# Kernel tuning notes

Hardware: AMD Instinct MI355X
Metric: run time of the kernel (lower is better)

Reference implementation:

```python
import jax, jax.numpy as jnp
import numpy as np

BATCH = 4096
NUM_INPUTS = 784
WIDTH = 16000        # neurons per logic layer, divisible by NUM_CLASSES
N_HIDDEN = 4         # width->width layers stacked for scan (plus the input layer)
NUM_CLASSES = 10


def setup_inputs() -> dict:
    key = jax.random.key(0)
    ks = jax.random.split(key, 7)
    x = jax.random.bernoulli(ks[0], 0.5, (BATCH, NUM_INPUTS))
    idx_a0 = jax.random.randint(ks[1], (WIDTH,), 0, NUM_INPUTS, dtype=jnp.int32)
    idx_b0 = jax.random.randint(ks[2], (WIDTH,), 0, NUM_INPUTS, dtype=jnp.int32)
    neg0 = jax.random.bernoulli(ks[3], 0.5, (WIDTH, 2))
    idx_a = jax.random.randint(ks[4], (N_HIDDEN, WIDTH), 0, WIDTH, dtype=jnp.int32)
    idx_b = jax.random.randint(ks[5], (N_HIDDEN, WIDTH), 0, WIDTH, dtype=jnp.int32)
    neg = jax.random.bernoulli(ks[6], 0.5, (N_HIDDEN, WIDTH, 2))
    return {"x": x, "idx_a0": idx_a0, "idx_b0": idx_b0, "neg0": neg0,
            "idx_a": idx_a, "idx_b": idx_b, "neg": neg}


def _gate(a, b, nf):
    # gate = (maybe-NOT a) AND (maybe-NOT b); NOT on booleans == XOR with flag
    return (a ^ nf[:, 0]) & (b ^ nf[:, 1])


def reference(x, idx_a0, idx_b0, neg0, idx_a, idx_b, neg):
    # input layer: gather wires from the boolean input
    h = _gate(x[:, idx_a0], x[:, idx_b0], neg0)  # [BATCH, WIDTH] bool

    def step(h, p):
        ia, ib, nf = p
        return _gate(h[:, ia], h[:, ib], nf), None

    h, _ = jax.lax.scan(step, h, (idx_a, idx_b, neg))
    # GroupSum: popcount per class group -> int32 logits
    out = h.reshape(BATCH, NUM_CLASSES, WIDTH // NUM_CLASSES).sum(-1, dtype=jnp.int32)
    return out
```

## Files before the change

### kernel.cpp

```cpp
#include <hip/hip_runtime.h>


#define NIN   784
#define WIDTH 16000
#define SW    16384
#define NH    4
#define NC    10
#define GPC   1600
#define NBLK  128
#define TPB   1024

typedef unsigned int u32;

__global__ void desc_kernel(const int* __restrict__ ia0, const int* __restrict__ ib0,
                            const int* __restrict__ n0,
                            const int* __restrict__ ia, const int* __restrict__ ib,
                            const int* __restrict__ n, u32* __restrict__ desc) {
    int t = blockIdx.x * blockDim.x + threadIdx.x;
    if (t >= (NH + 1) * SW) return;
    int l = t >> 14;
    int g = t & (SW - 1);
    u32 d = 0;
    if (g < WIDTH) {
        int a, b, na, nb;
        if (l == 0) { a = ia0[g]; b = ib0[g]; na = n0[2 * g]; nb = n0[2 * g + 1]; }
        else {
            int o = (l - 1) * WIDTH + g;
            a = ia[o]; b = ib[o]; na = n[2 * o]; nb = n[2 * o + 1];
        }
        d = (u32)a | ((u32)b << 14) | (na ? (1u << 28) : 0u) | (nb ? (1u << 29) : 0u);
    }
    desc[t] = d;
}

__launch_bounds__(TPB, 4)
__global__ void net_kernel(const int* __restrict__ x, const u32* __restrict__ desc,
                           int* __restrict__ out) {
    __shared__ __align__(16) u32 xw[NIN];
    __shared__ __align__(16) u32 bufA[SW];
    __shared__ __align__(16) u32 bufB[SW];

    int w = blockIdx.x;
    int t = threadIdx.x;

    uint4 dreg[4];
    {
        const uint4* d0 = (const uint4*)desc;
#pragma unroll
        for (int j = 0; j < 4; ++j) dreg[j] = d0[t + j * TPB];
    }

    if (t < NIN) {
        const int* base = x + (size_t)(w * 32) * NIN + t;
        u32 acc = 0;
#pragma unroll
        for (int r = 0; r < 32; ++r)
            acc |= (base[(size_t)r * NIN] != 0 ? 1u : 0u) << r;
        xw[t] = acc;
    }
    __syncthreads();

    u32* cur = xw;
#pragma unroll
    for (int l = 0; l <= NH; ++l) {
        u32* dst = (l & 1) ? bufB : bufA;
        uint4 dn[4];
        if (l < NH) {
            const uint4* dq = (const uint4*)(desc + (size_t)(l + 1) * SW);
#pragma unroll
            for (int j = 0; j < 4; ++j) dn[j] = dq[t + j * TPB];
        }
        u32 av[16], bv[16];
#pragma unroll
        for (int j = 0; j < 4; ++j) {
            u32 d0 = dreg[j].x, d1 = dreg[j].y, d2 = dreg[j].z, d3 = dreg[j].w;
            av[4 * j + 0] = cur[d0 & 0x3FFFu]; bv[4 * j + 0] = cur[(d0 >> 14) & 0x3FFFu];
            av[4 * j + 1] = cur[d1 & 0x3FFFu]; bv[4 * j + 1] = cur[(d1 >> 14) & 0x3FFFu];
            av[4 * j + 2] = cur[d2 & 0x3FFFu]; bv[4 * j + 2] = cur[(d2 >> 14) & 0x3FFFu];
            av[4 * j + 3] = cur[d3 & 0x3FFFu]; bv[4 * j + 3] = cur[(d3 >> 14) & 0x3FFFu];
        }
#pragma unroll
        for (int j = 0; j < 4; ++j) {
            u32 d0 = dreg[j].x, d1 = dreg[j].y, d2 = dreg[j].z, d3 = dreg[j].w;
            uint4 r;
            r.x = (av[4 * j + 0] ^ (0u - ((d0 >> 28) & 1u))) & (bv[4 * j + 0] ^ (0u - ((d0 >> 29) & 1u)));
            r.y = (av[4 * j + 1] ^ (0u - ((d1 >> 28) & 1u))) & (bv[4 * j + 1] ^ (0u - ((d1 >> 29) & 1u)));
            r.z = (av[4 * j + 2] ^ (0u - ((d2 >> 28) & 1u))) & (bv[4 * j + 2] ^ (0u - ((d2 >> 29) & 1u)));
            r.w = (av[4 * j + 3] ^ (0u - ((d3 >> 28) & 1u))) & (bv[4 * j + 3] ^ (0u - ((d3 >> 29) & 1u)));
            *(uint4*)(dst + 4 * (t + j * TPB)) = r;
        }
        __syncthreads();
#pragma unroll
        for (int j = 0; j < 4; ++j) dreg[j] = dn[j];
        cur = dst;
    }
    u32* res = bufA;

    int wave = t >> 6, lane = t & 63;
    if (wave < NC) {
        int c = wave;
        const u32* base = res + c * GPC;
        u32 p0 = 0, p1 = 0, p2 = 0, p3 = 0, p4 = 0;
#define CSA5(VAL) { u32 cy = (VAL); u32 s; \
        s = p0; p0 = s ^ cy; cy = s & cy; \
        s = p1; p1 = s ^ cy; cy = s & cy; \
        s = p2; p2 = s ^ cy; cy = s & cy; \
        s = p3; p3 = s ^ cy; cy = s & cy; \
        s = p4; p4 = s ^ cy; }
#pragma unroll
        for (int k = 0; k < 6; ++k) {
            uint4 v = *(const uint4*)(base + 4 * lane + 256 * k);
            CSA5(v.x); CSA5(v.y); CSA5(v.z); CSA5(v.w);
        }
        CSA5(base[1536 + lane]);
#undef CSA5

        u32 pl[11];
        pl[0] = p0; pl[1] = p1; pl[2] = p2; pl[3] = p3; pl[4] = p4;
#pragma unroll
        for (int s = 0; s < 6; ++s) {
            int np = 5 + s;
            u32 q[11];
#pragma unroll
            for (int i = 0; i < 11; ++i) if (i < np) q[i] = __shfl_xor(pl[i], 1 << s, 64);
            u32 carry = 0;
#pragma unroll
            for (int i = 0; i < 11; ++i) if (i < np) {
                u32 a = pl[i], b = q[i];
                u32 xr = a ^ b;
                pl[i] = xr ^ carry;
                carry = (a & b) | (carry & xr);
            }
            pl[np] = carry;
        }

        if (lane < 32) {
            int cntv = 0;
#pragma unroll
            for (int i = 0; i < 11; ++i) cntv += (int)((pl[i] >> lane) & 1u) << i;
            out[((size_t)w * 32 + lane) * NC + c] = cntv;
        }
    }
}

extern "C" void kernel_launch(void* const* d_in, const int* in_sizes, int n_in,
                              void* d_out, int out_size, void* d_ws, size_t ws_size,
                              hipStream_t stream) {
    const int* x      = (const int*)d_in[0];
    const int* idx_a0 = (const int*)d_in[1];
    const int* idx_b0 = (const int*)d_in[2];
    const int* neg0   = (const int*)d_in[3];
    const int* idx_a  = (const int*)d_in[4];
    const int* idx_b  = (const int*)d_in[5];
    const int* neg    = (const int*)d_in[6];
    int* out = (int*)d_out;

    u32* desc = (u32*)d_ws;

    int ndesc = (NH + 1) * SW;
    desc_kernel<<<(ndesc + 255) / 256, 256, 0, stream>>>(
        idx_a0, idx_b0, neg0, idx_a, idx_b, neg, desc);

    net_kernel<<<NBLK, TPB, 0, stream>>>(x, desc, out);
}
```

Measured before the change: 86.04 us.

## Swap gate operand order per wire to reduce LDS bank conflicts

Adds a preprocessing kernel that, for each wavefront-sized group of gate descriptors, tries several pseudo-random a/b operand swaps. It scores each candidate by the worst-case LDS bank collision count of the two gather loads and writes back the best one, swapping the negation flags along with the operands. Because AND is commutative the result is unchanged, while the shared-memory gathers in the main kernel should see fewer bank conflicts. The cost is an extra kernel launch with a 32-iteration ballot loop per candidate on every call.

```diff
diff --git a/kernel.cpp b/kernel.cpp
--- a/kernel.cpp
+++ b/kernel.cpp
@@ -9,8 +9,10 @@
 #define GPC   1600
 #define NBLK  128
 #define TPB   1024
+#define NGRP  (5 * 16 * 4 * 4)
 
 typedef unsigned int u32;
+typedef unsigned long long u64;
 
 __global__ void desc_kernel(const int* __restrict__ ia0, const int* __restrict__ ib0,
                             const int* __restrict__ n0,
@@ -33,6 +35,52 @@
     desc[t] = d;
 }
 
+__device__ __forceinline__ u32 hash3(u32 x) {
+    x ^= x >> 15; x *= 2246822519u; x ^= x >> 13; x *= 3266489917u; x ^= x >> 16;
+    return x;
+}
+
+__global__ void balance_kernel(u32* __restrict__ desc) {
+    int tid = blockIdx.x * blockDim.x + threadIdx.x;
+    int u = tid >> 6;
+    int lane = tid & 63;
+    if (u >= NGRP) return;
+    int e  = u & 3;
+    int j  = (u >> 2) & 3;
+    int wv = (u >> 4) & 15;
+    int l  = u >> 8;
+
+    int g = 4 * (wv * 64 + lane + 1024 * j) + e;
+    size_t idx = (size_t)l * SW + g;
+    u32 d = desc[idx];
+    u32 a = d & 0x3FFFu, b = (d >> 14) & 0x3FFFu;
+    u32 ba = a & 31u, bb = b & 31u;
+
+    u32 bestCost = ~0u;
+    int bestk = 0;
+#pragma unroll
+    for (int k = 0; k < 8; ++k) {
+        u32 sw = (k == 0) ? 0u : (hash3((u32)lane * 2654435761u ^ (u32)u * 40503u ^ (u32)k * 668265263u) & 1u);
+        u32 ka = sw ? bb : ba;
+        u32 kb = sw ? ba : bb;
+        u32 Ma = 0, Mb = 0;
+        for (u32 bank = 0; bank < 32; ++bank) {
+            u32 ca = (u32)__popcll(__ballot(ka == bank));
+            u32 cb = (u32)__popcll(__ballot(kb == bank));
+            Ma = Ma > ca ? Ma : ca;
+            Mb = Mb > cb ? Mb : cb;
+        }
+        u32 cost = Ma + Mb;
+        if (cost < bestCost) { bestCost = cost; bestk = k; }
+    }
+    u32 sw = (bestk == 0) ? 0u
+           : (hash3((u32)lane * 2654435761u ^ (u32)u * 40503u ^ (u32)bestk * 668265263u) & 1u);
+    if (sw) {
+        u32 na = (d >> 28) & 1u, nb = (d >> 29) & 1u;
+        desc[idx] = b | (a << 14) | (nb << 28) | (na << 29);
+    }
+}
+
 __launch_bounds__(TPB, 4)
 __global__ void net_kernel(const int* __restrict__ x, const u32* __restrict__ desc,
                            int* __restrict__ out) {
@@ -161,5 +209,7 @@
     desc_kernel<<<(ndesc + 255) / 256, 256, 0, stream>>>(
         idx_a0, idx_b0, neg0, idx_a, idx_b, neg, desc);
 
+    balance_kernel<<<(NGRP * 64) / 256, 256, 0, stream>>>(desc);
+
     net_kernel<<<NBLK, TPB, 0, stream>>>(x, desc, out);
 }
```

Measured after the change: 94.12 us. 1.09x slower.

## Split each batch word across two cooperating blocks with global-memory exchange

Applied to the files above, without the earlier changes.

Each 32-sample word is now handled by two blocks, each computing half of every layer's neurons. After each layer the halves are exchanged through a global staging buffer, with a flag-based spin wait between partner blocks, and the class popcount is split five and five. This doubles the block count to fill more CUs, at the cost of global memory traffic and a cross-block synchronisation per layer. It relies on partner blocks being co-resident, which is a deadlock risk if they are not.

```diff
diff --git a/kernel.cpp b/kernel.cpp
--- a/kernel.cpp
+++ b/kernel.cpp
@@ -7,8 +7,9 @@
 #define NH    4
 #define NC    10
 #define GPC   1600
-#define NBLK  128
+#define NBLK  256
 #define TPB   1024
+#define HALF  8192
 
 typedef unsigned int u32;
 
@@ -35,19 +36,25 @@
 
 __launch_bounds__(TPB, 4)
 __global__ void net_kernel(const int* __restrict__ x, const u32* __restrict__ desc,
-                           int* __restrict__ out) {
+                           int* __restrict__ out, u32* __restrict__ stage,
+                           u32* __restrict__ flags) {
     __shared__ __align__(16) u32 xw[NIN];
     __shared__ __align__(16) u32 bufA[SW];
     __shared__ __align__(16) u32 bufB[SW];
 
-    int w = blockIdx.x;
+    int bid = blockIdx.x;
+    int w = bid >> 1;
+    int h = bid & 1;
     int t = threadIdx.x;
 
-    uint4 dreg[4];
+    u32* flag_own = flags + 2 * w + h;
+    u32* flag_par = flags + 2 * w + (1 - h);
+
+    uint4 dreg[2];
     {
         const uint4* d0 = (const uint4*)desc;
-#pragma unroll
-        for (int j = 0; j < 4; ++j) dreg[j] = d0[t + j * TPB];
+        dreg[0] = d0[t + (2 * h + 0) * TPB];
+        dreg[1] = d0[t + (2 * h + 1) * TPB];
     }
 
     if (t < NIN) {
@@ -64,41 +71,68 @@
 #pragma unroll
     for (int l = 0; l <= NH; ++l) {
         u32* dst = (l & 1) ? bufB : bufA;
-        uint4 dn[4];
+        uint4 dn[2];
         if (l < NH) {
             const uint4* dq = (const uint4*)(desc + (size_t)(l + 1) * SW);
-#pragma unroll
-            for (int j = 0; j < 4; ++j) dn[j] = dq[t + j * TPB];
-        }
-        u32 av[16], bv[16];
-#pragma unroll
-        for (int j = 0; j < 4; ++j) {
-            u32 d0 = dreg[j].x, d1 = dreg[j].y, d2 = dreg[j].z, d3 = dreg[j].w;
-            av[4 * j + 0] = cur[d0 & 0x3FFFu]; bv[4 * j + 0] = cur[(d0 >> 14) & 0x3FFFu];
-            av[4 * j + 1] = cur[d1 & 0x3FFFu]; bv[4 * j + 1] = cur[(d1 >> 14) & 0x3FFFu];
-            av[4 * j + 2] = cur[d2 & 0x3FFFu]; bv[4 * j + 2] = cur[(d2 >> 14) & 0x3FFFu];
-            av[4 * j + 3] = cur[d3 & 0x3FFFu]; bv[4 * j + 3] = cur[(d3 >> 14) & 0x3FFFu];
-        }
-#pragma unroll
-        for (int j = 0; j < 4; ++j) {
-            u32 d0 = dreg[j].x, d1 = dreg[j].y, d2 = dreg[j].z, d3 = dreg[j].w;
+            dn[0] = dq[t + (2 * h + 0) * TPB];
+            dn[1] = dq[t + (2 * h + 1) * TPB];
+        }
+        u32 av[8], bv[8];
+#pragma unroll
+        for (int jl = 0; jl < 2; ++jl) {
+            av[4 * jl + 0] = cur[dreg[jl].x & 0x3FFFu];
+            av[4 * jl + 1] = cur[dreg[jl].y & 0x3FFFu];
+            av[4 * jl + 2] = cur[dreg[jl].z & 0x3FFFu];
+            av[4 * jl + 3] = cur[dreg[jl].w & 0x3FFFu];
+        }
+#pragma unroll
+        for (int jl = 0; jl < 2; ++jl) {
+            bv[4 * jl + 0] = cur[(dreg[jl].x >> 14) & 0x3FFFu];
+            bv[4 * jl + 1] = cur[(dreg[jl].y >> 14) & 0x3FFFu];
+            bv[4 * jl + 2] = cur[(dreg[jl].z >> 14) & 0x3FFFu];
+            bv[4 * jl + 3] = cur[(dreg[jl].w >> 14) & 0x3FFFu];
+        }
+        u32* stg = stage + (((size_t)(l & 1) * 128 + w) * 2 + h) * HALF;
+#pragma unroll
+        for (int jl = 0; jl < 2; ++jl) {
+            u32 d0 = dreg[jl].x, d1 = dreg[jl].y, d2 = dreg[jl].z, d3 = dreg[jl].w;
             uint4 r;
-            r.x = (av[4 * j + 0] ^ (0u - ((d0 >> 28) & 1u))) & (bv[4 * j + 0] ^ (0u - ((d0 >> 29) & 1u)));
-            r.y = (av[4 * j + 1] ^ (0u - ((d1 >> 28) & 1u))) & (bv[4 * j + 1] ^ (0u - ((d1 >> 29) & 1u)));
-            r.z = (av[4 * j + 2] ^ (0u - ((d2 >> 28) & 1u))) & (bv[4 * j + 2] ^ (0u - ((d2 >> 29) & 1u)));
-            r.w = (av[4 * j + 3] ^ (0u - ((d3 >> 28) & 1u))) & (bv[4 * j + 3] ^ (0u - ((d3 >> 29) & 1u)));
+            r.x = (av[4 * jl + 0] ^ (0u - ((d0 >> 28) & 1u))) & (bv[4 * jl + 0] ^ (0u - ((d0 >> 29) & 1u)));
+            r.y = (av[4 * jl + 1] ^ (0u - ((d1 >> 28) & 1u))) & (bv[4 * jl + 1] ^ (0u - ((d1 >> 29) & 1u)));
+            r.z = (av[4 * jl + 2] ^ (0u - ((d2 >> 28) & 1u))) & (bv[4 * jl + 2] ^ (0u - ((d2 >> 29) & 1u)));
+            r.w = (av[4 * jl + 3] ^ (0u - ((d3 >> 28) & 1u))) & (bv[4 * jl + 3] ^ (0u - ((d3 >> 29) & 1u)));
+            int j = 2 * h + jl;
             *(uint4*)(dst + 4 * (t + j * TPB)) = r;
+            *(uint4*)(stg + 4 * (t + jl * TPB)) = r;
         }
         __syncthreads();
-#pragma unroll
-        for (int j = 0; j < 4; ++j) dreg[j] = dn[j];
+        if (t == 0) {
+            __threadfence();
+            atomicAdd(flag_own, 1u);
+            while (__hip_atomic_load(flag_par, __ATOMIC_ACQUIRE,
+                                     __HIP_MEMORY_SCOPE_AGENT) < (u32)(l + 1)) {
+                __builtin_amdgcn_s_sleep(2);
+            }
+        }
+        __syncthreads();
+        {
+            const u32* ps = stage + (((size_t)(l & 1) * 128 + w) * 2 + (1 - h)) * HALF;
+#pragma unroll
+            for (int jl = 0; jl < 2; ++jl) {
+                uint4 v = *(const uint4*)(ps + 4 * (t + jl * TPB));
+                int j = 2 * (1 - h) + jl;
+                *(uint4*)(dst + 4 * (t + j * TPB)) = v;
+            }
+        }
+        __syncthreads();
+        dreg[0] = dn[0]; dreg[1] = dn[1];
         cur = dst;
     }
     u32* res = bufA;
 
     int wave = t >> 6, lane = t & 63;
-    if (wave < NC) {
-        int c = wave;
+    if (wave < 5) {
+        int c = 5 * h + wave;
         const u32* base = res + c * GPC;
         u32 p0 = 0, p1 = 0, p2 = 0, p3 = 0, p4 = 0;
 #define CSA5(VAL) { u32 cy = (VAL); u32 s; \
@@ -155,11 +189,16 @@
     const int* neg    = (const int*)d_in[6];
     int* out = (int*)d_out;
 
-    u32* desc = (u32*)d_ws;
+    char* ws    = (char*)d_ws;
+    u32*  desc  = (u32*)ws;
+    u32*  flags = (u32*)(ws + 327680);
+    u32*  stage = (u32*)(ws + 327680 + 4096);
+
+    hipMemsetAsync(flags, 0, 256 * sizeof(u32), stream);
 
     int ndesc = (NH + 1) * SW;
     desc_kernel<<<(ndesc + 255) / 256, 256, 0, stream>>>(
         idx_a0, idx_b0, neg0, idx_a, idx_b, neg, desc);
 
-    net_kernel<<<NBLK, TPB, 0, stream>>>(x, desc, out);
+    net_kernel<<<NBLK, TPB, 0, stream>>>(x, desc, out, stage, flags);
 }
```

After: 160.1 us. 1.86x slower.
